# Optimization experiments

Measured on AMD Instinct MI355X. Metric: run time of the kernel, lower is better.

Reference implementation:

```python
import jax, jax.numpy as jnp
import numpy as np

N, E, G = 50000, 800000, 512
F, DE, DG = 64, 16, 32
H, HEADS, C, L, NC = 128, 4, 32, 3, 1
EPS = 1e-5


def _bn(x, g, b, m, v):
    # eval-mode BatchNorm1d with running stats
    return (x - m) / jnp.sqrt(v + EPS) * g + b


def setup_inputs():
    key = jax.random.key(0)
    ks = jax.random.split(key, 24)

    def bn_params(k, d):
        k1, k2, k3, k4 = jax.random.split(k, 4)
        return (1.0 + 0.1 * jax.random.normal(k1, (d,), jnp.float32),
                0.1 * jax.random.normal(k2, (d,), jnp.float32),
                0.1 * jax.random.normal(k3, (d,), jnp.float32),
                jax.random.uniform(k4, (d,), jnp.float32, 0.5, 1.5))

    sc = lambda k, sh, fan: jax.random.normal(k, sh, jnp.float32) / np.float32(np.sqrt(fan))
    inp = {}
    inp['x'] = jax.random.normal(ks[0], (N, F), jnp.float32)
    inp['edge_attr'] = jax.random.normal(ks[1], (E, DE), jnp.float32)
    inp['global_features'] = jax.random.normal(ks[2], (G, DG), jnp.float32)
    inp['edge_index'] = jax.random.randint(ks[3], (2, E), 0, N)
    inp['batch'] = jnp.sort(jax.random.randint(ks[4], (N,), 0, G))
    inp['node_w'] = sc(ks[5], (F, H), F); inp['node_b'] = jnp.zeros((H,), jnp.float32)
    inp['node_bn_g'], inp['node_bn_b'], inp['node_bn_m'], inp['node_bn_v'] = bn_params(ks[6], H)
    inp['edge_w'] = sc(ks[7], (DE, H), DE); inp['edge_b'] = jnp.zeros((H,), jnp.float32)
    inp['glob_w'] = sc(ks[8], (DG, H), DG); inp['glob_b'] = jnp.zeros((H,), jnp.float32)
    inp['glob_bn_g'], inp['glob_bn_b'], inp['glob_bn_m'], inp['glob_bn_v'] = bn_params(ks[9], H)
    inp['gat_lin'] = sc(ks[10], (L, H, HEADS * C), H)
    inp['gat_asrc'] = sc(ks[11], (L, HEADS, C), C)
    inp['gat_adst'] = sc(ks[12], (L, HEADS, C), C)
    inp['gat_bias'] = jnp.zeros((L, H), jnp.float32)
    bg, bb, bm, bv = zip(*[bn_params(jax.random.fold_in(ks[13], i), H) for i in range(L)])
    inp['bn_g'] = jnp.stack(bg); inp['bn_b'] = jnp.stack(bb)
    inp['bn_m'] = jnp.stack(bm); inp['bn_v'] = jnp.stack(bv)
    inp['lin1_w'] = sc(ks[14], (3 * H, H), 3 * H); inp['lin1_b'] = jnp.zeros((H,), jnp.float32)
    inp['lin2_w'] = sc(ks[15], (H, NC), H); inp['lin2_b'] = jnp.zeros((NC,), jnp.float32)
    return inp


def reference(x, edge_attr, global_features, edge_index, batch, node_w, node_b, node_bn_g, node_bn_b, node_bn_m, node_bn_v, edge_w, edge_b, glob_w, glob_b, glob_bn_g, glob_bn_b, glob_bn_m, glob_bn_v, gat_lin, gat_asrc, gat_adst, gat_bias, bn_g, bn_b, bn_m, bn_v, lin1_w, lin1_b, lin2_w, lin2_b):
    n = x.shape[0]
    h = jax.nn.relu(_bn(x @ node_w + node_b, node_bn_g, node_bn_b, node_bn_m, node_bn_v))
    _ = jax.nn.relu(edge_attr @ edge_w + edge_b)  # edge encoder: computed but unused by GATConv, as in source
    # add self loops (PyG GATConv default)
    loops = jnp.arange(n)
    src = jnp.concatenate([edge_index[0], loops])
    dst = jnp.concatenate([edge_index[1], loops])
    for i in range(L):
        identity = h
        hh = (h @ gat_lin[i]).reshape(n, HEADS, C)
        a_src = jnp.einsum('nhc,hc->nh', hh, gat_asrc[i])
        a_dst = jnp.einsum('nhc,hc->nh', hh, gat_adst[i])
        e = jax.nn.leaky_relu(a_src[src] + a_dst[dst], 0.2)  # [E+n, HEADS]
        e_max = jax.ops.segment_max(e, dst, num_segments=n)
        ee = jnp.exp(e - e_max[dst])
        den = jax.ops.segment_sum(ee, dst, num_segments=n)
        alpha = ee / (den[dst] + 1e-16)
        out = jax.ops.segment_sum(hh[src] * alpha[..., None], dst, num_segments=n)
        out = out.reshape(n, HEADS * C) + gat_bias[i]
        out = jax.nn.relu(_bn(out, bn_g[i], bn_b[i], bn_m[i], bn_v[i]))
        h = out + identity  # residual: dims always match (HEADS*C == H)
    g = global_features.shape[0]
    cnt = jax.ops.segment_sum(jnp.ones((n,), h.dtype), batch, num_segments=g)
    x_mean = jax.ops.segment_sum(h, batch, num_segments=g) / jnp.maximum(cnt, 1.0)[:, None]
    x_max = jax.ops.segment_max(h, batch, num_segments=g)
    x_max = jnp.where(jnp.isfinite(x_max), x_max, 0.0)  # guard rare empty graphs
    gfeat = jax.nn.relu(_bn(global_features @ glob_w + glob_b, glob_bn_g, glob_bn_b, glob_bn_m, glob_bn_v))
    z = jnp.concatenate([x_mean, x_max, gfeat], axis=1)
    z = jax.nn.relu(z @ lin1_w + lin1_b)
    return z @ lin2_w + lin2_b
```

## Files before the change

### kernel.cpp

```cpp
#include <hip/hip_runtime.h>
#include <hip/hip_bf16.h>

typedef unsigned short u16;
typedef unsigned int   u32;
typedef unsigned long long u64;

#define HD 128
#define FD 64
#define EPS 1e-5f

using bf16x8 = __attribute__((ext_vector_type(8))) short;
using f32x4  = __attribute__((ext_vector_type(4))) float;

__device__ __forceinline__ float b2f(u16 v) { return __uint_as_float(((u32)v) << 16); }
__device__ __forceinline__ u16 f2b(float f) {
    u32 u = __float_as_uint(f);
    return (u16)((u + 0x7FFF + ((u >> 16) & 1)) >> 16);
}
__device__ __forceinline__ float lo16(u32 u) { return __uint_as_float(u << 16); }
__device__ __forceinline__ float hi16(u32 u) { return __uint_as_float(u & 0xFFFF0000u); }

__device__ __forceinline__ bf16x8 pack8(const float* p) {
    bf16x8 r;
    #pragma unroll
    for (int j = 0; j < 8; j++) r[j] = (short)f2b(p[j]);
    return r;
}

__global__ __launch_bounds__(256) void k_hist(const int* __restrict__ dst, int* __restrict__ cnt, int E) {
    int e = blockIdx.x * 256 + threadIdx.x;
    if (e < E) atomicAdd(&cnt[dst[e]], 1);
}

__global__ __launch_bounds__(256) void k_scanA(const int* __restrict__ cnt, int* __restrict__ rowptr,
                                               int* __restrict__ bsum, int N) {
    __shared__ int s[256];
    int tid = threadIdx.x;
    int i = blockIdx.x * 256 + tid;
    s[tid] = (i < N) ? cnt[i] : 0;
    __syncthreads();
    for (int off = 1; off < 256; off <<= 1) {
        int t = (tid >= off) ? s[tid - off] : 0;
        __syncthreads();
        s[tid] += t;
        __syncthreads();
    }
    if (i < N) rowptr[i + 1] = s[tid];
    if (tid == 255) bsum[blockIdx.x] = s[255];
}

__global__ __launch_bounds__(256) void k_scanB(int* __restrict__ bsum, int SB) {
    __shared__ int s[256];
    int tid = threadIdx.x;
    s[tid] = (tid < SB) ? bsum[tid] : 0;
    __syncthreads();
    for (int off = 1; off < 256; off <<= 1) {
        int t = (tid >= off) ? s[tid - off] : 0;
        __syncthreads();
        s[tid] += t;
        __syncthreads();
    }
    if (tid < SB) bsum[tid] = s[tid];
}

__global__ __launch_bounds__(256) void k_scanC(int* __restrict__ rowptr, const int* __restrict__ bsum, int N) {
    int i = blockIdx.x * 256 + threadIdx.x;
    if (i == 0) rowptr[0] = 0;
    if (i < N) {
        int b = i >> 8;
        if (b > 0) rowptr[i + 1] += bsum[b - 1];
    }
}

__global__ __launch_bounds__(256) void k_binA(
    const int* __restrict__ src, const int* __restrict__ dst, const int* __restrict__ rowptr,
    int* __restrict__ bcur, u64* __restrict__ binned, int E, int bsh, int NB, int numTiles) {
    __shared__ u32 os[4096], od[4096];
    __shared__ int hist[256], obase[256], ofs[256], gpos[256];
    int tid = threadIdx.x;
    for (int t = blockIdx.x; t < numTiles; t += gridDim.x) {
        int base = t * 4096;
        int cnt = E - base; if (cnt > 4096) cnt = 4096;
        hist[tid] = 0;
        __syncthreads();
        u32 rs[16], rd[16];
        #pragma unroll
        for (int r = 0; r < 16; r++) {
            int li = r * 256 + tid;
            if (li < cnt) {
                rs[r] = src[base + li];
                rd[r] = dst[base + li];
                atomicAdd(&hist[rd[r] >> bsh], 1);
            }
        }
        __syncthreads();
        int val = hist[tid];
        obase[tid] = val;
        __syncthreads();
        for (int off = 1; off < 256; off <<= 1) {
            int t2 = (tid >= off) ? obase[tid - off] : 0;
            __syncthreads();
            obase[tid] += t2;
            __syncthreads();
        }
        int excl = obase[tid] - val;
        __syncthreads();
        obase[tid] = excl;
        ofs[tid] = excl;
        __syncthreads();
        #pragma unroll
        for (int r = 0; r < 16; r++) {
            int li = r * 256 + tid;
            if (li < cnt) {
                int b = rd[r] >> bsh;
                int posn = atomicAdd(&ofs[b], 1);
                os[posn] = rs[r];
                od[posn] = rd[r];
            }
        }
        __syncthreads();
        if (tid < NB && hist[tid] > 0)
            gpos[tid] = rowptr[tid << bsh] + atomicAdd(&bcur[tid], hist[tid]);
        __syncthreads();
        for (int li = tid; li < cnt; li += 256) {
            u32 d = od[li];
            int b = d >> bsh;
            binned[(size_t)gpos[b] + (li - obase[b])] = ((u64)d << 32) | os[li];
        }
        __syncthreads();
    }
}

__global__ __launch_bounds__(256) void k_binB(
    const u64* __restrict__ binned, const int* __restrict__ rowptr,
    int* __restrict__ fill, int* __restrict__ colidx, int N, int bsh) {
    int b = blockIdx.x;
    int n0 = b << bsh;
    int n1 = (b + 1) << bsh; if (n1 > N) n1 = N;
    int r0 = rowptr[n0], r1 = rowptr[n1];
    for (int i = r0 + threadIdx.x; i < r1; i += 256) {
        u64 pk = binned[i];
        u32 d = (u32)(pk >> 32), s = (u32)pk;
        int slot = atomicAdd(&fill[d], 1);
        colidx[rowptr[d] + slot] = (int)s;
    }
}

__global__ __launch_bounds__(256) void k_wprep(const float* __restrict__ node_w, const float* __restrict__ gat_lin,
                                               u16* __restrict__ wf_node, u16* __restrict__ wf_gat) {
    int y = blockIdx.y;
    const float* src; u16* dst; int K;
    if (y == 0) { src = node_w; dst = wf_node; K = FD; }
    else { src = gat_lin + (size_t)(y - 1) * HD * HD; dst = wf_gat + (size_t)(y - 1) * HD * HD; K = HD; }
    int KT = K >> 5;
    int total = K * HD;
    for (int f = blockIdx.x * 256 + threadIdx.x; f < total; f += gridDim.x * 256) {
        int j = f & 7;
        int lane = (f >> 3) & 63;
        int t = f >> 9;
        int kt = t % KT;
        int ct = t / KT;
        int k = kt * 32 + (lane >> 4) * 8 + j;
        int col = ct * 16 + (lane & 15);
        dst[f] = f2b(src[k * HD + col]);
    }
}

__global__ __launch_bounds__(256) void k_node_mfma(
    const float* __restrict__ x, const u16* __restrict__ wf, const float* __restrict__ bias,
    const float* __restrict__ g, const float* __restrict__ bb, const float* __restrict__ m,
    const float* __restrict__ v, u16* __restrict__ h, int N) {
    int wv = threadIdx.x >> 6, lane = threadIdx.x & 63;
    int rowbase = blockIdx.x * 64 + wv * 16;
    if (rowbase >= N) return;
    int n16 = lane & 15, quad = lane >> 4;
    int arow = min(rowbase + n16, N - 1);
    f32x4 acc[8] = {};
    #pragma unroll
    for (int kt = 0; kt < 2; kt++) {
        bf16x8 a = pack8(x + (size_t)arow * FD + kt * 32 + quad * 8);
        #pragma unroll
        for (int ct = 0; ct < 8; ct++) {
            bf16x8 b = *(const bf16x8*)(wf + ((size_t)(ct * 2 + kt) * 64 + lane) * 8);
            acc[ct] = __builtin_amdgcn_mfma_f32_16x16x32_bf16(a, b, acc[ct], 0, 0, 0);
        }
    }
    #pragma unroll
    for (int ct = 0; ct < 8; ct++) {
        int col = ct * 16 + n16;
        float sc = g[col] * rsqrtf(v[col] + EPS);
        float bi = (bias[col] - m[col]) * sc + bb[col];
        #pragma unroll
        for (int reg = 0; reg < 4; reg++) {
            int row = rowbase + quad * 4 + reg;
            if (row < N) h[(size_t)row * HD + col] = f2b(fmaxf(acc[ct][reg] * sc + bi, 0.f));
        }
    }
}

__global__ __launch_bounds__(256) void k_gat_mfma(
    const u16* __restrict__ h, const u16* __restrict__ wf,
    const float* __restrict__ asrcw, const float* __restrict__ adstw,
    u16* __restrict__ hh, float* __restrict__ a_src, float* __restrict__ a_dst, int N) {
    int wv = threadIdx.x >> 6, lane = threadIdx.x & 63;
    int rowbase = blockIdx.x * 64 + wv * 16;
    if (rowbase >= N) return;
    int n16 = lane & 15, quad = lane >> 4;
    int arow = min(rowbase + n16, N - 1);
    f32x4 acc[8] = {};
    #pragma unroll
    for (int kt = 0; kt < 4; kt++) {
        bf16x8 a = *(const bf16x8*)(h + (size_t)arow * HD + kt * 32 + quad * 8);
        #pragma unroll
        for (int ct = 0; ct < 8; ct++) {
            bf16x8 b = *(const bf16x8*)(wf + ((size_t)(ct * 4 + kt) * 64 + lane) * 8);
            acc[ct] = __builtin_amdgcn_mfma_f32_16x16x32_bf16(a, b, acc[ct], 0, 0, 0);
        }
    }
    float asw[8], adw[8];
    #pragma unroll
    for (int ct = 0; ct < 8; ct++) {
        asw[ct] = asrcw[ct * 16 + n16];
        adw[ct] = adstw[ct * 16 + n16];
    }
    float ps[4][4], pd[4][4];
    #pragma unroll
    for (int hd = 0; hd < 4; hd++)
        #pragma unroll
        for (int reg = 0; reg < 4; reg++) {
            ps[hd][reg] = acc[2 * hd][reg] * asw[2 * hd] + acc[2 * hd + 1][reg] * asw[2 * hd + 1];
            pd[hd][reg] = acc[2 * hd][reg] * adw[2 * hd] + acc[2 * hd + 1][reg] * adw[2 * hd + 1];
        }
    #pragma unroll
    for (int msk = 1; msk < 16; msk <<= 1) {
        #pragma unroll
        for (int hd = 0; hd < 4; hd++)
            #pragma unroll
            for (int reg = 0; reg < 4; reg++) {
                ps[hd][reg] += __shfl_xor(ps[hd][reg], msk);
                pd[hd][reg] += __shfl_xor(pd[hd][reg], msk);
            }
    }
    #pragma unroll
    for (int reg = 0; reg < 4; reg++) {
        int row = rowbase + quad * 4 + reg;
        if (row < N) {
            #pragma unroll
            for (int ct = 0; ct < 8; ct++)
                hh[(size_t)row * HD + ct * 16 + n16] = f2b(acc[ct][reg]);
            if (n16 < 4) {
                float ws = 0.f, wd = 0.f;
                #pragma unroll
                for (int hd = 0; hd < 4; hd++)
                    if (n16 == hd) { ws = ps[hd][reg]; wd = pd[hd][reg]; }
                a_src[row * 4 + n16] = ws;
                a_dst[row * 4 + n16] = wd;
            }
        }
    }
}

__global__ __launch_bounds__(256) void k_agg(
    u16* __restrict__ h, const u32* __restrict__ hh32,
    const float* __restrict__ a_src, const float* __restrict__ a_dst,
    const int* __restrict__ rowptr, const int* __restrict__ colidx,
    const float* __restrict__ bias, const float* __restrict__ bng, const float* __restrict__ bnb,
    const float* __restrict__ bnm, const float* __restrict__ bnv, int N) {
    __shared__ int   sL[4][64];
    __shared__ __align__(16) float eeL[4][64][4];
    int wv = threadIdx.x >> 6, lane = threadIdx.x & 63;
    int node = blockIdx.x * 4 + wv;
    if (node >= N) return;
    int head = lane >> 4;
    const float4* as4p = (const float4*)a_src;
    float4 ad4 = ((const float4*)a_dst)[node];
    float adh = (head == 0) ? ad4.x : (head == 1) ? ad4.y : (head == 2) ? ad4.z : ad4.w;
    float ash = a_src[node * 4 + head];
    float e = ash + adh;
    e = (e > 0.f) ? e : 0.2f * e;
    float ee = __expf(e);
    float den = ee;
    u32 hv = hh32[(size_t)node * 64 + lane];
    float acc0 = ee * lo16(hv), acc1 = ee * hi16(hv);
    int beg = rowptr[node], end = rowptr[node + 1];
    for (int base = beg; base < end; base += 64) {
        int cnt = end - base; if (cnt > 64) cnt = 64;
        int s = 0;
        float4 e4 = {0.f, 0.f, 0.f, 0.f};
        if (lane < cnt) {
            s = colidx[base + lane];
            float4 as4 = as4p[s];
            float t0 = as4.x + ad4.x, t1 = as4.y + ad4.y, t2 = as4.z + ad4.z, t3 = as4.w + ad4.w;
            t0 = (t0 > 0.f) ? t0 : 0.2f * t0; t1 = (t1 > 0.f) ? t1 : 0.2f * t1;
            t2 = (t2 > 0.f) ? t2 : 0.2f * t2; t3 = (t3 > 0.f) ? t3 : 0.2f * t3;
            e4.x = __expf(t0); e4.y = __expf(t1); e4.z = __expf(t2); e4.w = __expf(t3);
        }
        sL[wv][lane] = s;
        ((float4*)eeL[wv][lane])[0] = e4;
        #pragma unroll 4
        for (int j = 0; j < cnt; j++) {
            int sj = sL[wv][j];
            float w = eeL[wv][j][head];
            u32 hv2 = hh32[(size_t)sj * 64 + lane];
            den += w;
            acc0 += w * lo16(hv2);
            acc1 += w * hi16(hv2);
        }
    }
    float inv = 1.0f / (den + 1e-16f);
    int c0 = lane * 2, c1 = c0 + 1;
    float o0 = acc0 * inv, o1 = acc1 * inv;
    float sc0 = bng[c0] * rsqrtf(bnv[c0] + EPS);
    float sc1 = bng[c1] * rsqrtf(bnv[c1] + EPS);
    o0 = (o0 + bias[c0] - bnm[c0]) * sc0 + bnb[c0];
    o1 = (o1 + bias[c1] - bnm[c1]) * sc1 + bnb[c1];
    o0 = fmaxf(o0, 0.f); o1 = fmaxf(o1, 0.f);
    u32 idv = ((const u32*)h)[(size_t)node * 64 + lane];
    o0 += lo16(idv); o1 += hi16(idv);
    ((u32*)h)[(size_t)node * 64 + lane] = ((u32)f2b(o1) << 16) | f2b(o0);
}

__global__ __launch_bounds__(256) void k_readout(
    const u16* __restrict__ h, const int* __restrict__ batch,
    const float* __restrict__ gf, const float* __restrict__ glob_w, const float* __restrict__ glob_b,
    const float* __restrict__ gbg, const float* __restrict__ gbb,
    const float* __restrict__ gbm, const float* __restrict__ gbv,
    const float* __restrict__ W1, const float* __restrict__ b1,
    const float* __restrict__ W2, const float* __restrict__ b2,
    float* __restrict__ out, int N, int G) {
    __shared__ float zs[384];
    __shared__ float sA[128], sB[128];
    __shared__ float pr[256];
    int g = blockIdx.x, tid = threadIdx.x;
    int c = tid & 127, half = tid >> 7;
    int lo = 0, hi = N;
    while (lo < hi) { int mid = (lo + hi) >> 1; if (batch[mid] < g) lo = mid + 1; else hi = mid; }
    int beg = lo;
    hi = N;
    while (lo < hi) { int mid = (lo + hi) >> 1; if (batch[mid] <= g) lo = mid + 1; else hi = mid; }
    int end = lo;
    float s = 0.f, mx = -3.4e38f;
    for (int r = beg + half; r < end; r += 2) {
        float v = b2f(h[(size_t)r * HD + c]);
        s += v; mx = fmaxf(mx, v);
    }
    if (half == 1) { sA[c] = s; sB[c] = mx; }
    __syncthreads();
    if (half == 0) {
        s += sA[c]; mx = fmaxf(mx, sB[c]);
        int cntn = end - beg;
        zs[c] = s / (float)(cntn > 0 ? cntn : 1);
        zs[128 + c] = (cntn == 0) ? 0.f : mx;
    } else {
        float acc = glob_b[c];
        #pragma unroll 8
        for (int k = 0; k < 32; k++) acc += gf[g * 32 + k] * glob_w[k * HD + c];
        float sc = gbg[c] * rsqrtf(gbv[c] + EPS);
        acc = (acc - gbm[c]) * sc + gbb[c];
        zs[256 + c] = fmaxf(acc, 0.f);
    }
    __syncthreads();
    float acc = (half == 0) ? b1[c] : 0.f;
    int k0 = half * 192;
    #pragma unroll 4
    for (int k = k0; k < k0 + 192; k++) acc += zs[k] * W1[k * HD + c];
    pr[tid] = acc;
    __syncthreads();
    if (half == 0) {
        float a = fmaxf(pr[c] + pr[c + 128], 0.f);
        pr[c] = a * W2[c];
    }
    __syncthreads();
    for (int sft = 64; sft > 0; sft >>= 1) {
        if (tid < sft) pr[tid] += pr[tid + sft];
        __syncthreads();
    }
    if (tid == 0) out[g] = pr[0] + b2[0];
}

extern "C" void kernel_launch(void* const* d_in, const int* in_sizes, int n_in,
                              void* d_out, int out_size, void* d_ws, size_t ws_size,
                              hipStream_t stream) {
    (void)n_in; (void)out_size; (void)ws_size;
    const float* x        = (const float*)d_in[0];
    const float* gfeat    = (const float*)d_in[2];
    const int*   ei       = (const int*)d_in[3];
    const int*   batch    = (const int*)d_in[4];
    const float* node_w   = (const float*)d_in[5];
    const float* node_b   = (const float*)d_in[6];
    const float* nbg      = (const float*)d_in[7];
    const float* nbb      = (const float*)d_in[8];
    const float* nbm      = (const float*)d_in[9];
    const float* nbv      = (const float*)d_in[10];
    const float* glob_w   = (const float*)d_in[13];
    const float* glob_b   = (const float*)d_in[14];
    const float* gbg      = (const float*)d_in[15];
    const float* gbb      = (const float*)d_in[16];
    const float* gbm      = (const float*)d_in[17];
    const float* gbv      = (const float*)d_in[18];
    const float* gat_lin  = (const float*)d_in[19];
    const float* gat_asrc = (const float*)d_in[20];
    const float* gat_adst = (const float*)d_in[21];
    const float* gat_bias = (const float*)d_in[22];
    const float* bn_g     = (const float*)d_in[23];
    const float* bn_b     = (const float*)d_in[24];
    const float* bn_m     = (const float*)d_in[25];
    const float* bn_v     = (const float*)d_in[26];
    const float* lin1_w   = (const float*)d_in[27];
    const float* lin1_b   = (const float*)d_in[28];
    const float* lin2_w   = (const float*)d_in[29];
    const float* lin2_b   = (const float*)d_in[30];

    const int N = in_sizes[0] / FD;
    const int E = in_sizes[3] / 2;
    const int G = in_sizes[2] / 32;
    const int* srcp = ei;
    const int* dstp = ei + E;

    int bsh = 8;
    while (((N + (1 << bsh) - 1) >> bsh) > 256) bsh++;
    const int NB = (N + (1 << bsh) - 1) >> bsh;

    char* p = (char*)d_ws;
    auto alloc = [&](size_t bytes) -> char* {
        char* r = p;
        p += (bytes + 255) & ~(size_t)255;
        return r;
    };
    u16*   h       = (u16*)alloc((size_t)N * HD * 2);
    u16*   hh      = (u16*)alloc((size_t)N * HD * 2);
    float* a_src   = (float*)alloc((size_t)N * 4 * 4);
    float* a_dst   = (float*)alloc((size_t)N * 4 * 4);
    int*   rowptr  = (int*)alloc((size_t)(N + 1) * 4);
    char*  zbase   = p;
    int*   cnt     = (int*)alloc((size_t)N * 4);
    int*   fill    = (int*)alloc((size_t)N * 4);
    int*   bcur    = (int*)alloc(256 * 4);
    size_t zbytes  = (size_t)(p - zbase);
    int*   bsum    = (int*)alloc(256 * 4);
    int*   colidx  = (int*)alloc((size_t)E * 4);
    u64*   binned  = (u64*)alloc((size_t)E * 8);
    u16*   wf_node = (u16*)alloc((size_t)FD * HD * 2);
    u16*   wf_gat  = (u16*)alloc((size_t)3 * HD * HD * 2);

    hipMemsetAsync(zbase, 0, zbytes, stream);

    k_wprep<<<dim3(32, 4), 256, 0, stream>>>(node_w, gat_lin, wf_node, wf_gat);

    int eb = (E + 255) / 256;
    int SB = (N + 255) / 256;
    k_hist<<<eb, 256, 0, stream>>>(dstp, cnt, E);
    k_scanA<<<SB, 256, 0, stream>>>(cnt, rowptr, bsum, N);
    k_scanB<<<1, 256, 0, stream>>>(bsum, SB);
    k_scanC<<<SB, 256, 0, stream>>>(rowptr, bsum, N);

    int numTiles = (E + 4095) / 4096;
    int binAGrid = numTiles < 512 ? numTiles : 512;
    k_binA<<<binAGrid, 256, 0, stream>>>(srcp, dstp, rowptr, bcur, binned, E, bsh, NB, numTiles);
    k_binB<<<NB, 256, 0, stream>>>(binned, rowptr, fill, colidx, N, bsh);

    k_node_mfma<<<(N + 63) / 64, 256, 0, stream>>>(x, wf_node, node_b, nbg, nbb, nbm, nbv, h, N);

    for (int i = 0; i < 3; i++) {
        k_gat_mfma<<<(N + 63) / 64, 256, 0, stream>>>(
            h, wf_gat + (size_t)i * HD * HD,
            gat_asrc + i * HD, gat_adst + i * HD,
            hh, a_src, a_dst, N);
        k_agg<<<(N + 3) / 4, 256, 0, stream>>>(
            h, (const u32*)hh, a_src, a_dst, rowptr, colidx,
            gat_bias + i * HD, bn_g + i * HD, bn_b + i * HD, bn_m + i * HD, bn_v + i * HD, N);
    }

    k_readout<<<G, 256, 0, stream>>>(h, batch, gfeat, glob_w, glob_b, gbg, gbb, gbm, gbv,
                                     lin1_w, lin1_b, lin2_w, lin2_b, (float*)d_out, N, G);
}
```

Baseline: 436.8 us.

## Split readout into pooling and batched MLP kernels with precomputed graph bounds

Graph segment boundaries are now computed once by a boundary-detection kernel instead of two binary searches per block. Pooling reads packed bf16 pairs across four waves, and the lin1/lin2 MLP moves to a separate kernel that processes 8 graphs per block with W1 staged in shared memory. Each graph block no longer reads the full 384x128 W1 matrix on its own. The cost is two extra launches and an intermediate z buffer in global memory.

```diff
diff --git a/kernel.cpp b/kernel.cpp
--- a/kernel.cpp
+++ b/kernel.cpp
@@ -69,6 +69,19 @@
     if (i < N) {
         int b = i >> 8;
         if (b > 0) rowptr[i + 1] += bsum[b - 1];
+    }
+}
+
+__global__ __launch_bounds__(256) void k_gbound(const int* __restrict__ batch, int* __restrict__ gs, int N, int G) {
+    int i = blockIdx.x * 256 + threadIdx.x;
+    if (i < N) {
+        int b = batch[i];
+        if (i == 0) { for (int g = 0; g <= b; g++) gs[g] = 0; }
+        else {
+            int pb = batch[i - 1];
+            for (int g = pb + 1; g <= b; g++) gs[g] = i;
+        }
+        if (i == N - 1) { for (int g = b + 1; g <= G; g++) gs[g] = N; }
     }
 }
 
@@ -320,62 +333,93 @@
     ((u32*)h)[(size_t)node * 64 + lane] = ((u32)f2b(o1) << 16) | f2b(o0);
 }
 
-__global__ __launch_bounds__(256) void k_readout(
-    const u16* __restrict__ h, const int* __restrict__ batch,
+__global__ __launch_bounds__(256) void k_pool(
+    const u16* __restrict__ h, const int* __restrict__ gs,
     const float* __restrict__ gf, const float* __restrict__ glob_w, const float* __restrict__ glob_b,
     const float* __restrict__ gbg, const float* __restrict__ gbb,
     const float* __restrict__ gbm, const float* __restrict__ gbv,
-    const float* __restrict__ W1, const float* __restrict__ b1,
-    const float* __restrict__ W2, const float* __restrict__ b2,
-    float* __restrict__ out, int N, int G) {
-    __shared__ float zs[384];
-    __shared__ float sA[128], sB[128];
-    __shared__ float pr[256];
+    float* __restrict__ z, int N, int G) {
+    __shared__ float s0L[4][64], s1L[4][64], m0L[4][64], m1L[4][64];
     int g = blockIdx.x, tid = threadIdx.x;
-    int c = tid & 127, half = tid >> 7;
-    int lo = 0, hi = N;
-    while (lo < hi) { int mid = (lo + hi) >> 1; if (batch[mid] < g) lo = mid + 1; else hi = mid; }
-    int beg = lo;
-    hi = N;
-    while (lo < hi) { int mid = (lo + hi) >> 1; if (batch[mid] <= g) lo = mid + 1; else hi = mid; }
-    int end = lo;
-    float s = 0.f, mx = -3.4e38f;
-    for (int r = beg + half; r < end; r += 2) {
-        float v = b2f(h[(size_t)r * HD + c]);
-        s += v; mx = fmaxf(mx, v);
-    }
-    if (half == 1) { sA[c] = s; sB[c] = mx; }
+    int wv = tid >> 6, lane = tid & 63;
+    int beg = gs[g], end = gs[g + 1];
+    const u32* h32 = (const u32*)h;
+    float s0 = 0.f, s1 = 0.f, m0 = -3.4e38f, m1 = -3.4e38f;
+    for (int r = beg + wv; r < end; r += 4) {
+        u32 pk = h32[(size_t)r * 64 + lane];
+        float v0 = lo16(pk), v1 = hi16(pk);
+        s0 += v0; s1 += v1;
+        m0 = fmaxf(m0, v0); m1 = fmaxf(m1, v1);
+    }
+    s0L[wv][lane] = s0; s1L[wv][lane] = s1;
+    m0L[wv][lane] = m0; m1L[wv][lane] = m1;
     __syncthreads();
-    if (half == 0) {
-        s += sA[c]; mx = fmaxf(mx, sB[c]);
-        int cntn = end - beg;
-        zs[c] = s / (float)(cntn > 0 ? cntn : 1);
-        zs[128 + c] = (cntn == 0) ? 0.f : mx;
-    } else {
+    if (tid < 64) {
+        float a0 = s0L[0][lane] + s0L[1][lane] + s0L[2][lane] + s0L[3][lane];
+        float a1 = s1L[0][lane] + s1L[1][lane] + s1L[2][lane] + s1L[3][lane];
+        float x0 = fmaxf(fmaxf(m0L[0][lane], m0L[1][lane]), fmaxf(m0L[2][lane], m0L[3][lane]));
+        float x1 = fmaxf(fmaxf(m1L[0][lane], m1L[1][lane]), fmaxf(m1L[2][lane], m1L[3][lane]));
+        int cnt = end - beg;
+        float inv = 1.0f / (float)(cnt > 0 ? cnt : 1);
+        if (cnt == 0) { x0 = 0.f; x1 = 0.f; }
+        ((float2*)(z + (size_t)g * 384))[lane] = make_float2(a0 * inv, a1 * inv);
+        ((float2*)(z + (size_t)g * 384 + 128))[lane] = make_float2(x0, x1);
+    } else if (tid >= 128) {
+        int c = tid - 128;
         float acc = glob_b[c];
         #pragma unroll 8
         for (int k = 0; k < 32; k++) acc += gf[g * 32 + k] * glob_w[k * HD + c];
         float sc = gbg[c] * rsqrtf(gbv[c] + EPS);
         acc = (acc - gbm[c]) * sc + gbb[c];
-        zs[256 + c] = fmaxf(acc, 0.f);
-    }
+        z[(size_t)g * 384 + 256 + c] = fmaxf(acc, 0.f);
+    }
+}
+
+__global__ __launch_bounds__(256) void k_lin(
+    const float* __restrict__ z, const float* __restrict__ W1, const float* __restrict__ b1,
+    const float* __restrict__ W2, const float* __restrict__ b2, float* __restrict__ out, int G) {
+    __shared__ float zL[8][384];
+    __shared__ float Wc[64][128];
+    __shared__ float red[8][128];
+    int tid = threadIdx.x;
+    int g0 = blockIdx.x * 8;
+    int c = tid & 127, half = tid >> 7;
+    for (int i = tid; i < 8 * 384; i += 256) {
+        int gi = i / 384, kk = i % 384;
+        zL[gi][kk] = (g0 + gi < G) ? z[(size_t)(g0 + gi) * 384 + kk] : 0.f;
+    }
+    float acc0 = 0.f, acc1 = 0.f, acc2 = 0.f, acc3 = 0.f;
+    int gb = half * 4;
+    for (int ch = 0; ch < 6; ch++) {
+        __syncthreads();
+        for (int i4 = tid; i4 < 2048; i4 += 256) {
+            int flat = i4 * 4;
+            int k = flat >> 7, cc = flat & 127;
+            *(float4*)&Wc[k][cc] = *(const float4*)&W1[(size_t)(ch * 64 + k) * HD + cc];
+        }
+        __syncthreads();
+        int kb = ch * 64;
+        #pragma unroll 4
+        for (int k = 0; k < 64; k++) {
+            float w = Wc[k][c];
+            acc0 += zL[gb + 0][kb + k] * w;
+            acc1 += zL[gb + 1][kb + k] * w;
+            acc2 += zL[gb + 2][kb + k] * w;
+            acc3 += zL[gb + 3][kb + k] * w;
+        }
+    }
+    float b1c = b1[c], w2c = W2[c];
     __syncthreads();
-    float acc = (half == 0) ? b1[c] : 0.f;
-    int k0 = half * 192;
-    #pragma unroll 4
-    for (int k = k0; k < k0 + 192; k++) acc += zs[k] * W1[k * HD + c];
-    pr[tid] = acc;
+    red[gb + 0][c] = fmaxf(acc0 + b1c, 0.f) * w2c;
+    red[gb + 1][c] = fmaxf(acc1 + b1c, 0.f) * w2c;
+    red[gb + 2][c] = fmaxf(acc2 + b1c, 0.f) * w2c;
+    red[gb + 3][c] = fmaxf(acc3 + b1c, 0.f) * w2c;
     __syncthreads();
-    if (half == 0) {
-        float a = fmaxf(pr[c] + pr[c + 128], 0.f);
-        pr[c] = a * W2[c];
-    }
-    __syncthreads();
-    for (int sft = 64; sft > 0; sft >>= 1) {
-        if (tid < sft) pr[tid] += pr[tid + sft];
-        __syncthreads();
-    }
-    if (tid == 0) out[g] = pr[0] + b2[0];
+    int gr = tid >> 5, l32 = tid & 31;
+    float v = red[gr][l32] + red[gr][l32 + 32] + red[gr][l32 + 64] + red[gr][l32 + 96];
+    #pragma unroll
+    for (int m = 1; m < 32; m <<= 1) v += __shfl_xor(v, m, 32);
+    if (l32 == 0 && g0 + gr < G) out[g0 + gr] = v + b2[0];
 }
 
 extern "C" void kernel_launch(void* const* d_in, const int* in_sizes, int n_in,
@@ -442,6 +486,8 @@
     u64*   binned  = (u64*)alloc((size_t)E * 8);
     u16*   wf_node = (u16*)alloc((size_t)FD * HD * 2);
     u16*   wf_gat  = (u16*)alloc((size_t)3 * HD * HD * 2);
+    float* z       = (float*)alloc((size_t)G * 384 * 4);
+    int*   gs      = (int*)alloc((size_t)(G + 1) * 4);
 
     hipMemsetAsync(zbase, 0, zbytes, stream);
 
@@ -453,6 +499,7 @@
     k_scanA<<<SB, 256, 0, stream>>>(cnt, rowptr, bsum, N);
     k_scanB<<<1, 256, 0, stream>>>(bsum, SB);
     k_scanC<<<SB, 256, 0, stream>>>(rowptr, bsum, N);
+    k_gbound<<<SB, 256, 0, stream>>>(batch, gs, N, G);
 
     int numTiles = (E + 4095) / 4096;
     int binAGrid = numTiles < 512 ? numTiles : 512;
@@ -471,6 +518,6 @@
             gat_bias + i * HD, bn_g + i * HD, bn_b + i * HD, bn_m + i * HD, bn_v + i * HD, N);
     }
 
-    k_readout<<<G, 256, 0, stream>>>(h, batch, gfeat, glob_w, glob_b, gbg, gbb, gbm, gbv,
-                                     lin1_w, lin1_b, lin2_w, lin2_b, (float*)d_out, N, G);
-}
+    k_pool<<<G, 256, 0, stream>>>(h, gs, gfeat, glob_w, glob_b, gbg, gbb, gbm, gbv, z, N, G);
+    k_lin<<<(G + 7) / 8, 256, 0, stream>>>(z, lin1_w, lin1_b, lin2_w, lin2_b, (float*)d_out, G);
+}
```

New measurement: 435.5 us. Within noise of the previous version (-0.3%).
